# Performance work log

Hardware: AMD Instinct MI355X
Metric: run time of the kernel (lower is better)

The kernel has to match this reference:

```python
import jax, jax.numpy as jnp
import numpy as np

N = 50000
E = 400000
F_IN = 5
H = 8
C1, C2, C3 = 64, 32, 16
NEG_SLOPE = 0.2


def setup_inputs() -> dict:
    key = jax.random.key(0)
    ks = jax.random.split(key, 16)
    s = 0.1  # small init scale
    return {
        "x": jax.random.normal(ks[0], (N, F_IN), jnp.float32),
        "edge_index": jax.random.randint(ks[1], (2, E), 0, N, jnp.int64),
        "edge_weight": jax.random.uniform(ks[2], (E,), jnp.float32),
        "W1": jax.random.normal(ks[3], (F_IN, H * C1), jnp.float32) * s,
        "a_src1": jax.random.normal(ks[4], (H, C1), jnp.float32) * s,
        "a_dst1": jax.random.normal(ks[5], (H, C1), jnp.float32) * s,
        "b1": jnp.zeros((H * C1,), jnp.float32),
        "W2": jax.random.normal(ks[6], (H * C1, H * C2), jnp.float32) * s,
        "a_src2": jax.random.normal(ks[7], (H, C2), jnp.float32) * s,
        "a_dst2": jax.random.normal(ks[8], (H, C2), jnp.float32) * s,
        "b2": jnp.zeros((H * C2,), jnp.float32),
        "Wg": jax.random.normal(ks[9], (H * C2, C3), jnp.float32) * s,
        "bg": jnp.zeros((C3,), jnp.float32),
        "Wfc": jax.random.normal(ks[10], (C3, 1), jnp.float32) * s,
        "bfc": jnp.zeros((1,), jnp.float32),
    }


def _gat_layer(x, W, a_src, a_dst, b, src, dst, n, heads, ch):
    # PyG GATConv (concat=True), eval mode (dropout off), self-loops already in src/dst.
    h = (x @ W).reshape(n, heads, ch)                      # (N, H, C)
    e_s = jnp.sum(h * a_src, axis=-1)                      # (N, H)
    e_d = jnp.sum(h * a_dst, axis=-1)                      # (N, H)
    e = jax.nn.leaky_relu(e_s[src] + e_d[dst], NEG_SLOPE)  # (Etot, H)
    m = jax.ops.segment_max(e, dst, num_segments=n)
    m = jnp.where(jnp.isfinite(m), m, 0.0)                 # guard empty segments
    ex = jnp.exp(e - m[dst])
    den = jax.ops.segment_sum(ex, dst, num_segments=n)
    alpha = ex / (den[dst] + 1e-16)                        # softmax over in-edges
    out = jax.ops.segment_sum(h[src] * alpha[..., None], dst, num_segments=n)
    return out.reshape(n, heads * ch) + b


def _gcn_layer(x, W, b, src, dst, w_full, n):
    # PyG GCNConv with gcn_norm: D^{-1/2} A_hat D^{-1/2}, self-loop weight 1.
    deg = jax.ops.segment_sum(w_full, dst, num_segments=n)
    dinv = jnp.where(deg > 0, jax.lax.rsqrt(deg), 0.0)
    norm = dinv[src] * w_full * dinv[dst]                  # (Etot,)
    h = x @ W                                              # (N, C3)
    out = jax.ops.segment_sum(h[src] * norm[:, None], dst, num_segments=n)
    return out + b


def reference(x, edge_index, edge_weight, W1, a_src1, a_dst1, b1,
              W2, a_src2, a_dst2, b2, Wg, bg, Wfc, bfc):
    n = x.shape[0]
    loops = jnp.arange(n, dtype=edge_index.dtype)
    src = jnp.concatenate([edge_index[0], loops])
    dst = jnp.concatenate([edge_index[1], loops])
    w_full = jnp.concatenate([edge_weight, jnp.ones((n,), edge_weight.dtype)])

    h = _gat_layer(x, W1, a_src1, a_dst1, b1, src, dst, n, H, C1)
    h = jax.nn.elu(h)
    h = _gat_layer(h, W2, a_src2, a_dst2, b2, src, dst, n, H, C2)
    h = jax.nn.elu(h)
    h = _gcn_layer(h, Wg, bg, src, dst, w_full, n)
    h = jax.nn.elu(h)
    out = jax.nn.sigmoid(h @ Wfc + bfc)                    # (N, 1)
    return out
```

## Files before the change

kernel.cpp:

```cpp
#include <hip/hip_runtime.h>
#include <hip/hip_bf16.h>
#include <float.h>
#include <math.h>

#define N_NODES 50000
#define N_EDGES 400000
#define ETOT    (N_EDGES + N_NODES)
#define F_IN    5
#define HEADS   8
#define C1      64
#define C2      32
#define C3      16
#define HC1     (HEADS * C1)
#define HC2     (HEADS * C2)
#define NEG_SLOPE 0.2f
#define NCHUNK  ((N_NODES + 255) / 256)
#define NH8     (N_NODES * HEADS)
#define MPAD    (((N_NODES + 63) / 64) * 64)
#define GCOLS   (HC2 + 16)
#define PACKBLK ((GCOLS * HC1) / 256)
#define SCATBLK ((ETOT + 255) / 256)
#define ES1BLK  ((NH8 + 255) / 256)
#define XPBLK   ((N_NODES * 8 + 255) / 256)
#define INIT_DEG  SCATBLK
#define INIT_XP   (INIT_DEG + XPBLK)
#define INIT_W2X  (INIT_XP + PACKBLK)
#define INIT_TOT  (INIT_W2X + ES1BLK)

typedef short bf16x8 __attribute__((ext_vector_type(8)));
typedef float f32x4  __attribute__((ext_vector_type(4)));
typedef unsigned short ushort_t;
typedef unsigned short ushort8_t __attribute__((ext_vector_type(8)));

__device__ __forceinline__ float eluf(float x) {
    return x > 0.f ? x : (expf(x) - 1.f);
}
__device__ __forceinline__ float bf2f(unsigned short u) {
    union { unsigned int i; float f; } v; v.i = ((unsigned int)u) << 16; return v.f;
}
__device__ __forceinline__ unsigned short f2bf(float f) {
    __hip_bfloat16 b = __float2bfloat16(f);
    return *(unsigned short*)&b;
}
__device__ __forceinline__ float softnum(float es, float ed) {
    float v = es + ed;
    v = v > 0.f ? v : NEG_SLOPE * v;
    return expf(v);
}

__global__ void k_init(const int* __restrict__ ei, const float* __restrict__ ew,
                       int* degi, float* degf,
                       const float* __restrict__ x, float* __restrict__ xp8,
                       const float* __restrict__ W2,
                       const float* __restrict__ a_src2, const float* __restrict__ a_dst2,
                       ushort_t* __restrict__ W2X,
                       const float* __restrict__ W1,
                       const float* __restrict__ a_src1, const float* __restrict__ a_dst1,
                       float* __restrict__ es, float* __restrict__ ed) {
    __shared__ float asl[HEADS * F_IN], adl[HEADS * F_IN];
    int b = blockIdx.x;
    int t = threadIdx.x;
    if (b < INIT_DEG) {
        int i = b * 256 + t;
        if (i >= ETOT) return;
        int d   = (i < N_EDGES) ? ei[N_EDGES + i] : (i - N_EDGES);
        float w = (i < N_EDGES) ? ew[i] : 1.f;
        atomicAdd(&degi[d], 1);
        atomicAdd(&degf[d], w);
    } else if (b < INIT_XP) {
        int g = (b - INIT_DEG) * 256 + t;
        if (g >= N_NODES * 8) return;
        int n = g >> 3, f = g & 7;
        xp8[g] = (f < F_IN) ? x[n * F_IN + f] : 0.f;
    } else if (b < INIT_W2X) {
        int idx = (b - INIT_XP) * 256 + t;
        int c = idx >> 9;
        int k = idx & 511;
        float v;
        if (c < HC2) {
            v = W2[(size_t)k * HC2 + c];
        } else {
            int h = (c - HC2) & 7;
            const float* av = (c < HC2 + 8) ? a_src2 : a_dst2;
            v = 0.f;
#pragma unroll 8
            for (int j = 0; j < C2; j++)
                v += W2[(size_t)k * HC2 + h * C2 + j] * av[h * C2 + j];
        }
        W2X[idx] = f2bf(v);
    } else {
        if (t < HEADS * F_IN) {
            int h = t / F_IN, f = t % F_IN;
            float s = 0.f, dv = 0.f;
            for (int c = 0; c < C1; c++) {
                float wv = W1[f * HC1 + h * C1 + c];
                s  += wv * a_src1[h * C1 + c];
                dv += wv * a_dst1[h * C1 + c];
            }
            asl[t] = s;
            adl[t] = dv;
        }
        __syncthreads();
        int g = (b - INIT_W2X) * 256 + t;
        if (g < NH8) {
            int n = g >> 3, h = g & 7;
            float vs = 0.f, vd = 0.f;
#pragma unroll
            for (int f = 0; f < F_IN; f++) {
                float xv = x[n * F_IN + f];
                vs += xv * asl[h * F_IN + f];
                vd += xv * adl[h * F_IN + f];
            }
            es[g] = vs;
            ed[g] = vd;
        }
    }
}

__global__ void k_scan_a(const int* __restrict__ deg, int* __restrict__ part) {
    __shared__ int lds[256];
    int t = threadIdx.x;
    int i = blockIdx.x * 256 + t;
    lds[t] = (i < N_NODES) ? deg[i] : 0;
    __syncthreads();
    for (int off = 128; off >= 1; off >>= 1) {
        if (t < off) lds[t] += lds[t + off];
        __syncthreads();
    }
    if (t == 0) part[blockIdx.x] = lds[0];
}

__global__ void k_scan_b(int* part) {
    __shared__ int lds[256];
    int t = threadIdx.x;
    int v = (t < NCHUNK) ? part[t] : 0;
    lds[t] = v;
    __syncthreads();
    for (int off = 1; off < 256; off <<= 1) {
        int x = (t >= off) ? lds[t - off] : 0;
        __syncthreads();
        lds[t] += x;
        __syncthreads();
    }
    if (t < NCHUNK) part[t] = lds[t] - v;
}

__global__ void k_scan_c(const int* __restrict__ deg, const int* __restrict__ part,
                         int* __restrict__ offs,
                         const float* __restrict__ degf, float* __restrict__ dinv) {
    __shared__ int lds[256];
    int t = threadIdx.x;
    int i = blockIdx.x * 256 + t;
    int v = (i < N_NODES) ? deg[i] : 0;
    lds[t] = v;
    __syncthreads();
    for (int off = 1; off < 256; off <<= 1) {
        int x = (t >= off) ? lds[t - off] : 0;
        __syncthreads();
        lds[t] += x;
        __syncthreads();
    }
    int excl = part[blockIdx.x] + lds[t] - v;
    if (i < N_NODES) {
        offs[i] = excl;
        float dd = degf[i];
        dinv[i] = dd > 0.f ? rsqrtf(dd) : 0.f;
    }
    if (i == N_NODES - 1) offs[N_NODES] = excl + v;
}

__global__ void k_scatter(const int* __restrict__ ei, const int* __restrict__ offs,
                          int* cursor, int2* __restrict__ csr,
                          const float* __restrict__ ew, const float* __restrict__ dinv) {
    int i = blockIdx.x * 256 + threadIdx.x;
    if (i >= ETOT) return;
    int s, d;
    float w;
    if (i < N_EDGES) { s = ei[i]; d = ei[N_EDGES + i]; w = ew[i]; }
    else             { s = d = i - N_EDGES; w = 1.f; }
    float nrm = dinv[s] * w * dinv[d];
    int pos = offs[d] + atomicAdd(&cursor[d], 1);
    csr[pos] = make_int2(s, __float_as_int(nrm));
}

__global__ __launch_bounds__(256) void k_aggexp(const float* __restrict__ xp8,
                                                const float* __restrict__ es1,
                                                const float* __restrict__ ed1,
                                                const int* __restrict__ offs,
                                                const int2* __restrict__ csr,
                                                const float* __restrict__ W1,
                                                const float* __restrict__ b1,
                                                ushort_t* __restrict__ x2bf) {
    __shared__ float ax[256 * F_IN];
    int t = threadIdx.x;
    int g = blockIdx.x * 256 + t;
    if (g < NH8) {
        int d = g >> 3, h = g & 7;
        float edv = ed1[g];
        int k0 = offs[d], k1 = offs[d + 1];
        float a0 = 0.f, a1 = 0.f, a2 = 0.f, a3 = 0.f, a4 = 0.f, exsum = 0.f;
        int k = k0;
        if (k + 1 < k1) {
            int2 c0 = csr[k], c1 = csr[k + 1];
            for (; k + 3 < k1; k += 2) {
                int2 n0 = csr[k + 2], n1 = csr[k + 3];
                float x0 = softnum(es1[c0.x * HEADS + h], edv);
                float x1 = softnum(es1[c1.x * HEADS + h], edv);
                float4 A0 = *(const float4*)(xp8 + (size_t)c0.x * 8);
                float  B0 = xp8[(size_t)c0.x * 8 + 4];
                float4 A1 = *(const float4*)(xp8 + (size_t)c1.x * 8);
                float  B1 = xp8[(size_t)c1.x * 8 + 4];
                a0 += x0 * A0.x + x1 * A1.x;
                a1 += x0 * A0.y + x1 * A1.y;
                a2 += x0 * A0.z + x1 * A1.z;
                a3 += x0 * A0.w + x1 * A1.w;
                a4 += x0 * B0   + x1 * B1;
                exsum += x0 + x1;
                c0 = n0; c1 = n1;
            }
            {
                float x0 = softnum(es1[c0.x * HEADS + h], edv);
                float x1 = softnum(es1[c1.x * HEADS + h], edv);
                float4 A0 = *(const float4*)(xp8 + (size_t)c0.x * 8);
                float  B0 = xp8[(size_t)c0.x * 8 + 4];
                float4 A1 = *(const float4*)(xp8 + (size_t)c1.x * 8);
                float  B1 = xp8[(size_t)c1.x * 8 + 4];
                a0 += x0 * A0.x + x1 * A1.x;
                a1 += x0 * A0.y + x1 * A1.y;
                a2 += x0 * A0.z + x1 * A1.z;
                a3 += x0 * A0.w + x1 * A1.w;
                a4 += x0 * B0   + x1 * B1;
                exsum += x0 + x1;
                k += 2;
            }
        }
        if (k < k1) {
            int2 c0 = csr[k];
            float x0 = softnum(es1[c0.x * HEADS + h], edv);
            float4 A0 = *(const float4*)(xp8 + (size_t)c0.x * 8);
            float  B0 = xp8[(size_t)c0.x * 8 + 4];
            a0 += x0 * A0.x;
            a1 += x0 * A0.y;
            a2 += x0 * A0.z;
            a3 += x0 * A0.w;
            a4 += x0 * B0;
            exsum += x0;
        }
        float inv = 1.f / (exsum + 1e-16f);
        float* ap = ax + t * F_IN;
        ap[0] = a0 * inv;
        ap[1] = a1 * inv;
        ap[2] = a2 * inv;
        ap[3] = a3 * inv;
        ap[4] = a4 * inv;
    }
    __syncthreads();
    int wave = t >> 6, j = t & 63;
    int n0 = blockIdx.x * 32;
    int h = j >> 3;
    const float* w1p = W1 + j * 8;
#pragma unroll 1
    for (int it = 0; it < 8; ++it) {
        int nl = wave * 8 + it;
        int n = n0 + nl;
        if (n >= N_NODES) break;
        const float* ap = ax + (nl * 8 + h) * F_IN;
        float av[F_IN];
#pragma unroll
        for (int f = 0; f < F_IN; f++) av[f] = ap[f];
        float4 s0 = *(const float4*)(b1 + j * 8);
        float4 s1 = *(const float4*)(b1 + j * 8 + 4);
#pragma unroll
        for (int f = 0; f < F_IN; f++) {
            float4 w0  = *(const float4*)(w1p + f * HC1);
            float4 w1v = *(const float4*)(w1p + f * HC1 + 4);
            s0.x += av[f] * w0.x;  s0.y += av[f] * w0.y;
            s0.z += av[f] * w0.z;  s0.w += av[f] * w0.w;
            s1.x += av[f] * w1v.x; s1.y += av[f] * w1v.y;
            s1.z += av[f] * w1v.z; s1.w += av[f] * w1v.w;
        }
        ushort8_t o;
        o[0] = f2bf(eluf(s0.x)); o[1] = f2bf(eluf(s0.y));
        o[2] = f2bf(eluf(s0.z)); o[3] = f2bf(eluf(s0.w));
        o[4] = f2bf(eluf(s1.x)); o[5] = f2bf(eluf(s1.y));
        o[6] = f2bf(eluf(s1.z)); o[7] = f2bf(eluf(s1.w));
        *(ushort8_t*)(x2bf + (size_t)n * HC1 + j * 8) = o;
    }
}

__global__ __launch_bounds__(256, 3) void k_gemm_mfma(const short* __restrict__ A,
                                                      const short* __restrict__ W2X,
                                                      ushort_t* __restrict__ h2bf,
                                                      float* __restrict__ es2,
                                                      float* __restrict__ ed2) {
    __shared__ short Bs[GCOLS * 32];
    int t    = threadIdx.x;
    int wave = t >> 6;
    int lane = t & 63;
    int lo   = lane & 15;
    int quad = lane >> 4;
    int m0   = blockIdx.x * 64 + wave * 16;
    const short* ap = A + (size_t)(m0 + lo) * HC1 + quad * 8;

    f32x4 acc[17];
#pragma unroll
    for (int f = 0; f < 17; f++) acc[f] = (f32x4){0.f, 0.f, 0.f, 0.f};

    for (int idx = t; idx < GCOLS * 4; idx += 256) {
        int c = idx >> 2, q = idx & 3;
        int s = (q + c + (c >> 2)) & 3;
        *(bf16x8*)(Bs + c * 32 + s * 8) = *(const bf16x8*)(W2X + (size_t)c * HC1 + q * 8);
    }
    __syncthreads();

#pragma unroll 1
    for (int k0 = 0; k0 < HC1; k0 += 32) {
        int nk = k0 + 32;
        bf16x8 pre[5];
        if (nk < HC1) {
#pragma unroll
            for (int j = 0; j < 5; j++) {
                int idx = t + j * 256;
                if (idx < GCOLS * 4) {
                    int c = idx >> 2, q = idx & 3;
                    pre[j] = *(const bf16x8*)(W2X + (size_t)c * HC1 + nk + q * 8);
                }
            }
        }
        bf16x8 aF = *(const bf16x8*)(ap + k0);
#pragma unroll
        for (int f = 0; f < 17; f++) {
            int c = f * 16 + lo;
            int s = (quad + c + (c >> 2)) & 3;
            bf16x8 bF = *(const bf16x8*)(Bs + c * 32 + s * 8);
            acc[f] = __builtin_amdgcn_mfma_f32_16x16x32_bf16(aF, bF, acc[f], 0, 0, 0);
        }
        __syncthreads();
        if (nk < HC1) {
#pragma unroll
            for (int j = 0; j < 5; j++) {
                int idx = t + j * 256;
                if (idx < GCOLS * 4) {
                    int c = idx >> 2, q = idx & 3;
                    int s = (q + c + (c >> 2)) & 3;
                    *(bf16x8*)(Bs + c * 32 + s * 8) = pre[j];
                }
            }
            __syncthreads();
        }
    }

    int rowb = m0 + quad * 4;
#pragma unroll
    for (int f = 0; f < 16; f++) {
#pragma unroll
        for (int r = 0; r < 4; r++) {
            int row = rowb + r;
            if (row < N_NODES)
                h2bf[(size_t)row * HC2 + f * 16 + lo] = f2bf(acc[f][r]);
        }
    }
#pragma unroll
    for (int r = 0; r < 4; r++) {
        int row = rowb + r;
        if (row < N_NODES) {
            if (lo < 8) es2[row * HEADS + lo]       = acc[16][r];
            else        ed2[row * HEADS + (lo - 8)] = acc[16][r];
        }
    }
}

__global__ __launch_bounds__(128) void k_gat_agg2(const ushort_t* __restrict__ h2bf,
                                                  const float* __restrict__ es2,
                                                  const float* __restrict__ ed2,
                                                  const int* __restrict__ offs,
                                                  const int2* __restrict__ csr,
                                                  const float* __restrict__ b2,
                                                  ushort_t* __restrict__ x3bf) {
    int wave = threadIdx.x >> 6;
    int lane = threadIdx.x & 63;
    int d = blockIdx.x * 2 + wave;
    if (d >= N_NODES) return;
    int c4 = lane * 4;
    int h  = lane >> 3;
    float edv = ed2[d * HEADS + h];
    int k0 = offs[d], k1 = offs[d + 1];
    float acc0 = 0.f, acc1 = 0.f, acc2 = 0.f, acc3 = 0.f, exsum = 0.f;
    int k = k0;
    for (; k + 3 < k1; k += 4) {
        int2 e0 = csr[k], e1 = csr[k + 1], e2 = csr[k + 2], e3 = csr[k + 3];
        float r0 = es2[e0.x * HEADS + h];
        float r1 = es2[e1.x * HEADS + h];
        float r2 = es2[e2.x * HEADS + h];
        float r3 = es2[e3.x * HEADS + h];
        ushort4 v0 = *(const ushort4*)(h2bf + (size_t)e0.x * HC2 + c4);
        ushort4 v1 = *(const ushort4*)(h2bf + (size_t)e1.x * HC2 + c4);
        ushort4 v2 = *(const ushort4*)(h2bf + (size_t)e2.x * HC2 + c4);
        ushort4 v3 = *(const ushort4*)(h2bf + (size_t)e3.x * HC2 + c4);
        float x0 = softnum(r0, edv);
        float x1 = softnum(r1, edv);
        float x2 = softnum(r2, edv);
        float x3 = softnum(r3, edv);
        acc0 += x0 * bf2f(v0.x) + x1 * bf2f(v1.x) + x2 * bf2f(v2.x) + x3 * bf2f(v3.x);
        acc1 += x0 * bf2f(v0.y) + x1 * bf2f(v1.y) + x2 * bf2f(v2.y) + x3 * bf2f(v3.y);
        acc2 += x0 * bf2f(v0.z) + x1 * bf2f(v1.z) + x2 * bf2f(v2.z) + x3 * bf2f(v3.z);
        acc3 += x0 * bf2f(v0.w) + x1 * bf2f(v1.w) + x2 * bf2f(v2.w) + x3 * bf2f(v3.w);
        exsum += (x0 + x1) + (x2 + x3);
    }
    for (; k < k1; k++) {
        int2 e0 = csr[k];
        float x0 = softnum(es2[e0.x * HEADS + h], edv);
        ushort4 v0 = *(const ushort4*)(h2bf + (size_t)e0.x * HC2 + c4);
        acc0 += x0 * bf2f(v0.x);
        acc1 += x0 * bf2f(v0.y);
        acc2 += x0 * bf2f(v0.z);
        acc3 += x0 * bf2f(v0.w);
        exsum += x0;
    }
    float inv = 1.f / (exsum + 1e-16f);
    float4 bias = *(const float4*)(b2 + c4);
    ushort4 o;
    o.x = f2bf(eluf(acc0 * inv + bias.x));
    o.y = f2bf(eluf(acc1 * inv + bias.y));
    o.z = f2bf(eluf(acc2 * inv + bias.z));
    o.w = f2bf(eluf(acc3 * inv + bias.w));
    *(ushort4*)(x3bf + (size_t)d * HC2 + c4) = o;
}

__global__ __launch_bounds__(256) void k_hg(const ushort_t* __restrict__ x3bf,
                                            const float* __restrict__ Wg,
                                            float* __restrict__ hg) {
    __shared__ float xs[16 * 260];
    int n0 = blockIdx.x * 16;
    int t  = threadIdx.x;
    for (int q = t; q < 16 * HC2 / 4; q += 256) {
        int r  = q >> 6;
        int cc = (q & 63) * 4;
        int n  = n0 + r;
        ushort4 v = make_ushort4(0, 0, 0, 0);
        if (n < N_NODES) v = *(const ushort4*)(x3bf + (size_t)n * HC2 + cc);
        xs[r * 260 + cc + 0] = bf2f(v.x);
        xs[r * 260 + cc + 1] = bf2f(v.y);
        xs[r * 260 + cc + 2] = bf2f(v.z);
        xs[r * 260 + cc + 3] = bf2f(v.w);
    }
    __syncthreads();
    int r = t >> 4, c = t & 15;
    const float* xr = xs + r * 260;
    float acc = 0.f;
#pragma unroll 8
    for (int k = 0; k < HC2; k += 4) {
        float4 v = *(const float4*)(xr + k);
        acc += v.x * Wg[(k + 0) * C3 + c];
        acc += v.y * Wg[(k + 1) * C3 + c];
        acc += v.z * Wg[(k + 2) * C3 + c];
        acc += v.w * Wg[(k + 3) * C3 + c];
    }
    int n = n0 + r;
    if (n < N_NODES) hg[(size_t)n * C3 + c] = acc;
}

__global__ __launch_bounds__(256) void k_gcn_out(const float* __restrict__ hg,
                                                 const int* __restrict__ offs,
                                                 const int2* __restrict__ csr,
                                                 const float* __restrict__ bg,
                                                 const float* __restrict__ Wfc,
                                                 const float* __restrict__ bfc,
                                                 float* __restrict__ out) {
    int t = threadIdx.x;
    int r = t >> 4, c = t & 15;
    int d = blockIdx.x * 16 + r;
    float val = 0.f;
    if (d < N_NODES) {
        int k0 = offs[d], k1 = offs[d + 1];
        float acc = 0.f;
        int k = k0;
        if (k + 1 < k1) {
            int2 e0 = csr[k], e1 = csr[k + 1];
            for (; k + 3 < k1; k += 2) {
                int2 n0 = csr[k + 2], n1 = csr[k + 3];
                acc += hg[(size_t)e0.x * C3 + c] * __int_as_float(e0.y);
                acc += hg[(size_t)e1.x * C3 + c] * __int_as_float(e1.y);
                e0 = n0; e1 = n1;
            }
            acc += hg[(size_t)e0.x * C3 + c] * __int_as_float(e0.y);
            acc += hg[(size_t)e1.x * C3 + c] * __int_as_float(e1.y);
            k += 2;
        }
        if (k < k1) {
            int2 e0 = csr[k];
            acc += hg[(size_t)e0.x * C3 + c] * __int_as_float(e0.y);
        }
        val = eluf(acc + bg[c]);
    }
    float z = val * Wfc[c];
#pragma unroll
    for (int off = 8; off >= 1; off >>= 1) z += __shfl_xor(z, off, 16);
    if (c == 0 && d < N_NODES) out[d] = 1.f / (1.f + expf(-(z + bfc[0])));
}

extern "C" void kernel_launch(void* const* d_in, const int* in_sizes, int n_in,
                              void* d_out, int out_size, void* d_ws, size_t ws_size,
                              hipStream_t stream) {
    const float* x       = (const float*)d_in[0];
    const int*   ei      = (const int*)  d_in[1];
    const float* ew      = (const float*)d_in[2];
    const float* W1      = (const float*)d_in[3];
    const float* a_src1  = (const float*)d_in[4];
    const float* a_dst1  = (const float*)d_in[5];
    const float* b1      = (const float*)d_in[6];
    const float* W2      = (const float*)d_in[7];
    const float* a_src2  = (const float*)d_in[8];
    const float* a_dst2  = (const float*)d_in[9];
    const float* b2      = (const float*)d_in[10];
    const float* Wg      = (const float*)d_in[11];
    const float* bg      = (const float*)d_in[12];
    const float* Wfc     = (const float*)d_in[13];
    const float* bfc     = (const float*)d_in[14];
    float* out = (float*)d_out;

    char* w = (char*)d_ws;
    size_t off = 0;
    auto alloc = [&](size_t bytes) -> void* {
        void* p = w + off;
        off = (off + bytes + 255) & ~(size_t)255;
        return p;
    };
    ushort_t* x2bf = (ushort_t*)alloc((size_t)MPAD * HC1 * 2);
    ushort_t* W2X  = (ushort_t*)alloc((size_t)GCOLS * HC1 * 2);
    ushort_t* h2bf = (ushort_t*)alloc((size_t)N_NODES * HC2 * 2);
    ushort_t* x3bf = (ushort_t*)alloc((size_t)N_NODES * HC2 * 2);
    float* hg     = (float*)alloc((size_t)N_NODES * C3 * 4);
    float* es1    = (float*)alloc((size_t)NH8 * 4);
    float* ed1    = (float*)alloc((size_t)NH8 * 4);
    float* es2    = (float*)alloc((size_t)NH8 * 4);
    float* ed2    = (float*)alloc((size_t)NH8 * 4);
    float* degf   = (float*)alloc((size_t)N_NODES * 4);
    int*   degi   = (int*)  alloc((size_t)N_NODES * 4);
    int*   cursor = (int*)  alloc((size_t)N_NODES * 4);
    char*  zero_end = w + off;
    int*   offs   = (int*)  alloc((size_t)(N_NODES + 1) * 4);
    int*   part   = (int*)  alloc(256 * 4);
    int2*  csr    = (int2*) alloc((size_t)ETOT * 8);
    float* dinv   = (float*)alloc((size_t)N_NODES * 4);
    float* xp8    = (float*)alloc((size_t)N_NODES * 8 * 4);

    hipMemsetAsync(degf, 0, (size_t)(zero_end - (char*)degf), stream);
    k_init<<<dim3(INIT_TOT), dim3(256), 0, stream>>>(
        ei, ew, degi, degf, x, xp8, W2, a_src2, a_dst2, W2X,
        W1, a_src1, a_dst1, es1, ed1);
    k_scan_a<<<dim3(NCHUNK), dim3(256), 0, stream>>>(degi, part);
    k_scan_b<<<dim3(1), dim3(256), 0, stream>>>(part);
    k_scan_c<<<dim3(NCHUNK), dim3(256), 0, stream>>>(degi, part, offs, degf, dinv);
    k_scatter<<<dim3(SCATBLK), dim3(256), 0, stream>>>(ei, offs, cursor, csr, ew, dinv);

    k_aggexp<<<dim3(ES1BLK), dim3(256), 0, stream>>>(
        xp8, es1, ed1, offs, csr, W1, b1, x2bf);

    k_gemm_mfma<<<dim3(MPAD / 64), dim3(256), 0, stream>>>(
        (const short*)x2bf, (const short*)W2X, h2bf, es2, ed2);
    k_gat_agg2<<<dim3((N_NODES + 1) / 2), dim3(128), 0, stream>>>(
        h2bf, es2, ed2, offs, csr, b2, x3bf);

    k_hg<<<dim3((N_NODES + 15) / 16), dim3(256), 0, stream>>>(x3bf, Wg, hg);
    k_gcn_out<<<dim3((N_NODES + 15) / 16), dim3(256), 0, stream>>>(
        hg, offs, csr, bg, Wfc, bfc, out);
}
```

Baseline: 310.4 us.

## Pack degree count and fixed-point weight into one 64-bit atomic, reuse rank

The separate int count and float weight-sum atomics are merged into a single 64-bit atomicAdd per edge, with the count in the high bits and the weight as fixed-point in the low bits. The returned old value gives each edge's rank within its destination, which is stored and reused in the scatter kernel in place of a second cursor atomic pass. The xp8 padding copy is folded into the es/ed block of the init kernel, dropping a separate block range. The weighted degree now carries fixed-point rounding, and ranks are stored as 16-bit values, which assumes in-degree below 65536.

```diff
diff --git a/kernel.cpp b/kernel.cpp
--- a/kernel.cpp
+++ b/kernel.cpp
@@ -21,11 +21,12 @@
 #define PACKBLK ((GCOLS * HC1) / 256)
 #define SCATBLK ((ETOT + 255) / 256)
 #define ES1BLK  ((NH8 + 255) / 256)
-#define XPBLK   ((N_NODES * 8 + 255) / 256)
 #define INIT_DEG  SCATBLK
-#define INIT_XP   (INIT_DEG + XPBLK)
-#define INIT_W2X  (INIT_XP + PACKBLK)
+#define INIT_W2X  (INIT_DEG + PACKBLK)
 #define INIT_TOT  (INIT_W2X + ES1BLK)
+
+#define WFIX_SCALE 68719476736.0f
+#define WFIX_MASK  ((1ULL << 46) - 1)
 
 typedef short bf16x8 __attribute__((ext_vector_type(8)));
 typedef float f32x4  __attribute__((ext_vector_type(4)));
@@ -49,7 +50,8 @@
 }
 
 __global__ void k_init(const int* __restrict__ ei, const float* __restrict__ ew,
-                       int* degi, float* degf,
+                       unsigned long long* __restrict__ pack,
+                       ushort_t* __restrict__ rank,
                        const float* __restrict__ x, float* __restrict__ xp8,
                        const float* __restrict__ W2,
                        const float* __restrict__ a_src2, const float* __restrict__ a_dst2,
@@ -63,17 +65,16 @@
     if (b < INIT_DEG) {
         int i = b * 256 + t;
         if (i >= ETOT) return;
-        int d   = (i < N_EDGES) ? ei[N_EDGES + i] : (i - N_EDGES);
-        float w = (i < N_EDGES) ? ew[i] : 1.f;
-        atomicAdd(&degi[d], 1);
-        atomicAdd(&degf[d], w);
-    } else if (b < INIT_XP) {
-        int g = (b - INIT_DEG) * 256 + t;
-        if (g >= N_NODES * 8) return;
-        int n = g >> 3, f = g & 7;
-        xp8[g] = (f < F_IN) ? x[n * F_IN + f] : 0.f;
+        int d;
+        float w;
+        if (i < N_EDGES) { d = ei[N_EDGES + i]; w = ew[i]; }
+        else             { d = i - N_EDGES;     w = 1.f; }
+        unsigned long long enc =
+            (1ULL << 46) | (unsigned long long)(w * WFIX_SCALE + 0.5f);
+        unsigned long long old = atomicAdd(&pack[d], enc);
+        rank[i] = (ushort_t)(old >> 46);
     } else if (b < INIT_W2X) {
-        int idx = (b - INIT_XP) * 256 + t;
+        int idx = (b - INIT_DEG) * 256 + t;
         int c = idx >> 9;
         int k = idx & 511;
         float v;
@@ -113,15 +114,17 @@
             }
             es[g] = vs;
             ed[g] = vd;
-        }
-    }
-}
-
-__global__ void k_scan_a(const int* __restrict__ deg, int* __restrict__ part) {
+            xp8[g] = (h < F_IN) ? x[n * F_IN + h] : 0.f;
+        }
+    }
+}
+
+__global__ void k_scan_a(const unsigned long long* __restrict__ pack,
+                         int* __restrict__ part) {
     __shared__ int lds[256];
     int t = threadIdx.x;
     int i = blockIdx.x * 256 + t;
-    lds[t] = (i < N_NODES) ? deg[i] : 0;
+    lds[t] = (i < N_NODES) ? (int)(pack[i] >> 46) : 0;
     __syncthreads();
     for (int off = 128; off >= 1; off >>= 1) {
         if (t < off) lds[t] += lds[t + off];
@@ -145,13 +148,14 @@
     if (t < NCHUNK) part[t] = lds[t] - v;
 }
 
-__global__ void k_scan_c(const int* __restrict__ deg, const int* __restrict__ part,
-                         int* __restrict__ offs,
-                         const float* __restrict__ degf, float* __restrict__ dinv) {
+__global__ void k_scan_c(const unsigned long long* __restrict__ pack,
+                         const int* __restrict__ part,
+                         int* __restrict__ offs, float* __restrict__ dinv) {
     __shared__ int lds[256];
     int t = threadIdx.x;
     int i = blockIdx.x * 256 + t;
-    int v = (i < N_NODES) ? deg[i] : 0;
+    unsigned long long p = (i < N_NODES) ? pack[i] : 0ULL;
+    int v = (int)(p >> 46);
     lds[t] = v;
     __syncthreads();
     for (int off = 1; off < 256; off <<= 1) {
@@ -163,14 +167,14 @@
     int excl = part[blockIdx.x] + lds[t] - v;
     if (i < N_NODES) {
         offs[i] = excl;
-        float dd = degf[i];
-        dinv[i] = dd > 0.f ? rsqrtf(dd) : 0.f;
+        float ws = (float)(p & WFIX_MASK) * (1.0f / WFIX_SCALE);
+        dinv[i] = ws > 0.f ? rsqrtf(ws) : 0.f;
     }
     if (i == N_NODES - 1) offs[N_NODES] = excl + v;
 }
 
 __global__ void k_scatter(const int* __restrict__ ei, const int* __restrict__ offs,
-                          int* cursor, int2* __restrict__ csr,
+                          const ushort_t* __restrict__ rank, int2* __restrict__ csr,
                           const float* __restrict__ ew, const float* __restrict__ dinv) {
     int i = blockIdx.x * 256 + threadIdx.x;
     if (i >= ETOT) return;
@@ -179,7 +183,7 @@
     if (i < N_EDGES) { s = ei[i]; d = ei[N_EDGES + i]; w = ew[i]; }
     else             { s = d = i - N_EDGES; w = 1.f; }
     float nrm = dinv[s] * w * dinv[d];
-    int pos = offs[d] + atomicAdd(&cursor[d], 1);
+    int pos = offs[d] + (int)rank[i];
     csr[pos] = make_int2(s, __float_as_int(nrm));
 }
 
@@ -535,24 +539,23 @@
     float* ed1    = (float*)alloc((size_t)NH8 * 4);
     float* es2    = (float*)alloc((size_t)NH8 * 4);
     float* ed2    = (float*)alloc((size_t)NH8 * 4);
-    float* degf   = (float*)alloc((size_t)N_NODES * 4);
-    int*   degi   = (int*)  alloc((size_t)N_NODES * 4);
-    int*   cursor = (int*)  alloc((size_t)N_NODES * 4);
+    unsigned long long* pack = (unsigned long long*)alloc((size_t)N_NODES * 8);
     char*  zero_end = w + off;
+    ushort_t* rank = (ushort_t*)alloc((size_t)ETOT * 2);
     int*   offs   = (int*)  alloc((size_t)(N_NODES + 1) * 4);
     int*   part   = (int*)  alloc(256 * 4);
     int2*  csr    = (int2*) alloc((size_t)ETOT * 8);
     float* dinv   = (float*)alloc((size_t)N_NODES * 4);
     float* xp8    = (float*)alloc((size_t)N_NODES * 8 * 4);
 
-    hipMemsetAsync(degf, 0, (size_t)(zero_end - (char*)degf), stream);
+    hipMemsetAsync(pack, 0, (size_t)(zero_end - (char*)pack), stream);
     k_init<<<dim3(INIT_TOT), dim3(256), 0, stream>>>(
-        ei, ew, degi, degf, x, xp8, W2, a_src2, a_dst2, W2X,
+        ei, ew, pack, rank, x, xp8, W2, a_src2, a_dst2, W2X,
         W1, a_src1, a_dst1, es1, ed1);
-    k_scan_a<<<dim3(NCHUNK), dim3(256), 0, stream>>>(degi, part);
+    k_scan_a<<<dim3(NCHUNK), dim3(256), 0, stream>>>(pack, part);
     k_scan_b<<<dim3(1), dim3(256), 0, stream>>>(part);
-    k_scan_c<<<dim3(NCHUNK), dim3(256), 0, stream>>>(degi, part, offs, degf, dinv);
-    k_scatter<<<dim3(SCATBLK), dim3(256), 0, stream>>>(ei, offs, cursor, csr, ew, dinv);
+    k_scan_c<<<dim3(NCHUNK), dim3(256), 0, stream>>>(pack, part, offs, dinv);
+    k_scatter<<<dim3(SCATBLK), dim3(256), 0, stream>>>(ei, offs, rank, csr, ew, dinv);
 
     k_aggexp<<<dim3(ES1BLK), dim3(256), 0, stream>>>(
         xp8, es1, ed1, offs, csr, W1, b1, x2bf);
```

Result: faster. 279.3 us (-10.0%).
